# Performance work log

Measured on AMD Instinct MI355X. Metric: run time of the kernel, lower is better.

## Reference

```python
import jax, jax.numpy as jnp
import numpy as np

POOL = 7              # roi_size (output bins per side)
SAMPLING_RATIO = 2    # bilinear samples per bin side
POOLED_DIM = 5        # CEM_FILTER(245) // (7*7)
SPATIAL_SCALE = 0.0625  # 1/16 feature stride


def setup_inputs() -> dict:
    key = jax.random.key(0)
    k1, k2, k3 = jax.random.split(key, 3)
    B, C, H, W = 8, 245, 100, 100
    N = 512
    IMG = 1600.0
    x = jax.random.normal(k1, (B, C, H, W), dtype=jnp.float32)
    xy = jax.random.uniform(k2, (B, N, 2), minval=0.0, maxval=IMG - 256.0)
    wh = jax.random.uniform(k3, (B, N, 2), minval=16.0, maxval=256.0)
    boxes = jnp.concatenate([xy, xy + wh], axis=-1)  # (x1,y1,x2,y2) in image coords
    return {"x": x, "boxes": boxes}


def reference(x, boxes):
    """Position-sensitive RoIAlign (torchvision ps_roi_align semantics).
    x: [B, C=POOLED_DIM*POOL*POOL, H, W]; boxes: [B, N, 4] in image coords.
    Returns [B*N, POOLED_DIM, POOL, POOL]."""
    B, C, H, W = x.shape
    Bb, N, _ = boxes.shape
    R = Bb * N
    g, P, D, s = SAMPLING_RATIO, POOL, POOLED_DIM, SPATIAL_SCALE

    batch_idx = jnp.repeat(jnp.arange(Bb, dtype=jnp.int32), N)  # convert_to_roi_format ids
    rois = boxes.reshape(R, 4)

    # aligned roi coords on the feature map (half-pixel offset)
    start_w = rois[:, 0] * s - 0.5
    start_h = rois[:, 1] * s - 0.5
    end_w = rois[:, 2] * s - 0.5
    end_h = rois[:, 3] * s - 0.5
    bin_h = (end_h - start_h) / P
    bin_w = (end_w - start_w) / P

    p = jnp.arange(P, dtype=jnp.float32)
    i = jnp.arange(g, dtype=jnp.float32)
    # sample coordinates, shape [R, P, g]
    ys = start_h[:, None, None] + p[None, :, None] * bin_h[:, None, None] \
         + (i[None, None, :] + 0.5) * bin_h[:, None, None] / g
    xs = start_w[:, None, None] + p[None, :, None] * bin_w[:, None, None] \
         + (i[None, None, :] + 0.5) * bin_w[:, None, None] / g

    # zero outside [-1, H] / [-1, W] (torchvision bilinear_interpolate)
    vy = ((ys >= -1.0) & (ys <= H)).astype(x.dtype)  # [R,P,g]
    vx = ((xs >= -1.0) & (xs <= W)).astype(x.dtype)

    yc = jnp.clip(ys, 0.0, H - 1.0)
    xc = jnp.clip(xs, 0.0, W - 1.0)
    yl = jnp.floor(yc).astype(jnp.int32)
    xl = jnp.floor(xc).astype(jnp.int32)
    yh = jnp.minimum(yl + 1, H - 1)
    xh = jnp.minimum(xl + 1, W - 1)
    ly = yc - yl.astype(x.dtype); hy = 1.0 - ly
    lx = xc - xl.astype(x.dtype); hx = 1.0 - lx

    # position-sensitive input channel: c_in = (d*P + ph)*P + pw, shape [D,P,P]
    c_in = ((jnp.arange(D)[:, None, None] * P + jnp.arange(P)[None, :, None]) * P
            + jnp.arange(P)[None, None, :]).astype(jnp.int32)

    # broadcast to [R, D, P(h), P(w), g(h), g(w)]
    b = batch_idx[:, None, None, None, None, None]
    c = c_in[None, :, :, :, None, None]
    gy = lambda a: a[:, None, :, None, :, None]  # y-axis arrays [R,P,g]
    gx = lambda a: a[:, None, None, :, None, :]  # x-axis arrays [R,P,g]

    v11 = x[b, c, gy(yl), gx(xl)]
    v12 = x[b, c, gy(yl), gx(xh)]
    v21 = x[b, c, gy(yh), gx(xl)]
    v22 = x[b, c, gy(yh), gx(xh)]
    val = (gy(hy) * gx(hx) * v11 + gy(hy) * gx(lx) * v12
           + gy(ly) * gx(hx) * v21 + gy(ly) * gx(lx) * v22)
    val = val * (gy(vy) * gx(vx))
    out = val.sum(axis=(4, 5)) / (g * g)  # average over sampling grid -> [R, D, P, P]
    return out
```

## Files before the change

kernel.cpp:

```cpp
#include <hip/hip_runtime.h>

#define POOL 7
#define SCALE 0.0625f
#define HW 10000
#define NROI 512
#define NCH 245

typedef const __attribute__((address_space(1))) void* gas_ptr;
typedef __attribute__((address_space(3))) void* las_ptr;

__global__ __launch_bounds__(512) void psroi_kernel(
    const float* __restrict__ x, const float* __restrict__ boxes,
    float* __restrict__ out, int H, int W)
{
    __shared__ float plane[HW + 4];

    int bid = blockIdx.x;
    int b = bid & 7;
    int c = bid >> 3;
    int p = b * NCH + c;
    int ph = (c / POOL) % POOL;
    int pw = c % POOL;

    int n = threadIdx.x;
    int r = b * NROI + n;

    float4 bx = *(const float4*)(boxes + (size_t)r * 4);

    const float4* __restrict__ src4 = (const float4*)(x + (size_t)p * HW);
    int lane = threadIdx.x & 63;
    int wave = threadIdx.x >> 6;
    #pragma unroll
    for (int i = 0; i < 5; ++i) {
        int chunk_base = i * 512 + wave * 64;
        int chunk = chunk_base + lane;
        if (chunk < HW / 4) {
            __builtin_amdgcn_global_load_lds(
                (gas_ptr)(src4 + chunk),
                (las_ptr)((char*)plane + (size_t)chunk_base * 16),
                16, 0, 0);
        }
    }
    if (threadIdx.x < 4) plane[HW + threadIdx.x] = 0.f;

    float sw = bx.x * SCALE - 0.5f;
    float sh = bx.y * SCALE - 0.5f;
    float ew = bx.z * SCALE - 0.5f;
    float eh = bx.w * SCALE - 0.5f;
    float bin_h = (eh - sh) / (float)POOL;
    float bin_w = (ew - sw) / (float)POOL;
    float fy0 = sh + (float)ph * bin_h;
    float fx0 = sw + (float)pw * bin_w;

    int   rowa[2], rstep[2];
    float wyh[2], wyl[2];
    #pragma unroll
    for (int iy = 0; iy < 2; ++iy) {
        float y  = fy0 + ((float)iy + 0.5f) * bin_h * 0.5f;
        float vy = (y >= -1.0f && y <= (float)H) ? 1.0f : 0.0f;
        float yc = fminf(fmaxf(y, 0.0f), (float)(H - 1));
        int   yl = (int)floorf(yc);
        float ly = yc - (float)yl;
        wyl[iy] = ly * vy;
        wyh[iy] = (1.0f - ly) * vy;
        rowa[iy]  = yl * W;
        rstep[iy] = (yl < H - 1) ? W : 0;
    }
    int   colx[2];
    float wxh[2], wxl[2];
    #pragma unroll
    for (int ix = 0; ix < 2; ++ix) {
        float xf = fx0 + ((float)ix + 0.5f) * bin_w * 0.5f;
        float vx = (xf >= -1.0f && xf <= (float)W) ? 1.0f : 0.0f;
        float xc = fminf(fmaxf(xf, 0.0f), (float)(W - 1));
        int   xl = (int)floorf(xc);
        float lx = xc - (float)xl;
        wxl[ix] = lx * vx;
        wxh[ix] = (1.0f - lx) * vx;
        colx[ix] = xl;
    }

    __syncthreads();

    float sum = 0.f;
    #pragma unroll
    for (int iy = 0; iy < 2; ++iy) {
        #pragma unroll
        for (int ix = 0; ix < 2; ++ix) {
            int a0 = rowa[iy] + colx[ix];
            int a1 = a0 + rstep[iy];
            float v11 = plane[a0];
            float v12 = plane[a0 + 1];
            float v21 = plane[a1];
            float v22 = plane[a1 + 1];
            float top = wxh[ix] * v11 + wxl[ix] * v12;
            float bot = wxh[ix] * v21 + wxl[ix] * v22;
            sum = fmaf(wyh[iy], top, sum);
            sum = fmaf(wyl[iy], bot, sum);
        }
    }
    out[(size_t)r * NCH + c] = sum * 0.25f;
}

extern "C" void kernel_launch(void* const* d_in, const int* in_sizes, int n_in,
                              void* d_out, int out_size, void* d_ws, size_t ws_size,
                              hipStream_t stream) {
    const float* x     = (const float*)d_in[0];
    const float* boxes = (const float*)d_in[1];
    float* out = (float*)d_out;

    const int H = 100, W = 100;
    (void)in_sizes; (void)n_in; (void)out_size; (void)d_ws; (void)ws_size;

    hipLaunchKernelGGL(psroi_kernel, dim3(NCH * 8), dim3(512), 0, stream,
                       x, boxes, out, H, W);
}
```

Baseline: 19.20 us.

## Process several channel planes per block with double-buffered LDS staging

```diff
diff --git a/kernel.cpp b/kernel.cpp
--- a/kernel.cpp
+++ b/kernel.cpp
@@ -5,101 +5,121 @@
 #define HW 10000
 #define NROI 512
 #define NCH 245
+#define JJ 64
 
 typedef const __attribute__((address_space(1))) void* gas_ptr;
 typedef __attribute__((address_space(3))) void* las_ptr;
 
 __global__ __launch_bounds__(512) void psroi_kernel(
     const float* __restrict__ x, const float* __restrict__ boxes,
-    float* __restrict__ out, int H, int W)
+    float* __restrict__ out)
 {
-    __shared__ float plane[HW + 4];
+    __shared__ float plane[2][HW + 4];
 
+    const int H = 100, W = 100;
     int bid = blockIdx.x;
     int b = bid & 7;
-    int c = bid >> 3;
-    int p = b * NCH + c;
-    int ph = (c / POOL) % POOL;
-    int pw = c % POOL;
+    int j = bid >> 3;
+    int npl = (j < 53) ? 4 : 3;
 
     int n = threadIdx.x;
     int r = b * NROI + n;
+    int lane = threadIdx.x & 63;
+    int wave = threadIdx.x >> 6;
+
+    const float* xb = x + (size_t)b * NCH * HW;
+
+    auto stage = [&](int buf, int c) {
+        const float4* src4 = (const float4*)(xb + (size_t)c * HW);
+        #pragma unroll
+        for (int i = 0; i < 5; ++i) {
+            int chunk_base = i * 512 + wave * 64;
+            int chunk = chunk_base + lane;
+            if (chunk < HW / 4) {
+                __builtin_amdgcn_global_load_lds(
+                    (gas_ptr)(src4 + chunk),
+                    (las_ptr)((char*)&plane[buf][0] + (size_t)chunk_base * 16),
+                    16, 0, 0);
+            }
+        }
+    };
 
     float4 bx = *(const float4*)(boxes + (size_t)r * 4);
-
-    const float4* __restrict__ src4 = (const float4*)(x + (size_t)p * HW);
-    int lane = threadIdx.x & 63;
-    int wave = threadIdx.x >> 6;
-    #pragma unroll
-    for (int i = 0; i < 5; ++i) {
-        int chunk_base = i * 512 + wave * 64;
-        int chunk = chunk_base + lane;
-        if (chunk < HW / 4) {
-            __builtin_amdgcn_global_load_lds(
-                (gas_ptr)(src4 + chunk),
-                (las_ptr)((char*)plane + (size_t)chunk_base * 16),
-                16, 0, 0);
-        }
-    }
-    if (threadIdx.x < 4) plane[HW + threadIdx.x] = 0.f;
+    stage(0, j);
+    if (threadIdx.x < 8)
+        plane[threadIdx.x >> 2][HW + (threadIdx.x & 3)] = 0.f;
 
     float sw = bx.x * SCALE - 0.5f;
     float sh = bx.y * SCALE - 0.5f;
-    float ew = bx.z * SCALE - 0.5f;
-    float eh = bx.w * SCALE - 0.5f;
-    float bin_h = (eh - sh) / (float)POOL;
-    float bin_w = (ew - sw) / (float)POOL;
-    float fy0 = sh + (float)ph * bin_h;
-    float fx0 = sw + (float)pw * bin_w;
-
-    int   rowa[2], rstep[2];
-    float wyh[2], wyl[2];
-    #pragma unroll
-    for (int iy = 0; iy < 2; ++iy) {
-        float y  = fy0 + ((float)iy + 0.5f) * bin_h * 0.5f;
-        float vy = (y >= -1.0f && y <= (float)H) ? 1.0f : 0.0f;
-        float yc = fminf(fmaxf(y, 0.0f), (float)(H - 1));
-        int   yl = (int)floorf(yc);
-        float ly = yc - (float)yl;
-        wyl[iy] = ly * vy;
-        wyh[iy] = (1.0f - ly) * vy;
-        rowa[iy]  = yl * W;
-        rstep[iy] = (yl < H - 1) ? W : 0;
-    }
-    int   colx[2];
-    float wxh[2], wxl[2];
-    #pragma unroll
-    for (int ix = 0; ix < 2; ++ix) {
-        float xf = fx0 + ((float)ix + 0.5f) * bin_w * 0.5f;
-        float vx = (xf >= -1.0f && xf <= (float)W) ? 1.0f : 0.0f;
-        float xc = fminf(fmaxf(xf, 0.0f), (float)(W - 1));
-        int   xl = (int)floorf(xc);
-        float lx = xc - (float)xl;
-        wxl[ix] = lx * vx;
-        wxh[ix] = (1.0f - lx) * vx;
-        colx[ix] = xl;
-    }
+    float bin_h = (bx.w * SCALE - 0.5f - sh) / (float)POOL;
+    float bin_w = (bx.z * SCALE - 0.5f - sw) / (float)POOL;
 
     __syncthreads();
 
-    float sum = 0.f;
-    #pragma unroll
-    for (int iy = 0; iy < 2; ++iy) {
+    for (int t = 0; t < npl; ++t) {
+        int c = j + JJ * t;
+        bool pre = (t + 1 < npl);
+        if (pre) stage((t + 1) & 1, j + JJ * (t + 1));
+
+        int ph = (c / POOL) % POOL;
+        int pw = c % POOL;
+        float fy0 = sh + (float)ph * bin_h;
+        float fx0 = sw + (float)pw * bin_w;
+
+        int   rowa[2], rstep[2];
+        float wyh[2], wyl[2];
+        #pragma unroll
+        for (int iy = 0; iy < 2; ++iy) {
+            float y  = fy0 + ((float)iy + 0.5f) * bin_h * 0.5f;
+            float vy = (y >= -1.0f && y <= (float)H) ? 1.0f : 0.0f;
+            float yc = fminf(fmaxf(y, 0.0f), (float)(H - 1));
+            int   yl = (int)floorf(yc);
+            float ly = yc - (float)yl;
+            wyl[iy] = ly * vy;
+            wyh[iy] = (1.0f - ly) * vy;
+            rowa[iy]  = yl * W;
+            rstep[iy] = (yl < H - 1) ? W : 0;
+        }
+        int   colx[2];
+        float wxh[2], wxl[2];
         #pragma unroll
         for (int ix = 0; ix < 2; ++ix) {
-            int a0 = rowa[iy] + colx[ix];
-            int a1 = a0 + rstep[iy];
-            float v11 = plane[a0];
-            float v12 = plane[a0 + 1];
-            float v21 = plane[a1];
-            float v22 = plane[a1 + 1];
-            float top = wxh[ix] * v11 + wxl[ix] * v12;
-            float bot = wxh[ix] * v21 + wxl[ix] * v22;
-            sum = fmaf(wyh[iy], top, sum);
-            sum = fmaf(wyl[iy], bot, sum);
+            float xf = fx0 + ((float)ix + 0.5f) * bin_w * 0.5f;
+            float vx = (xf >= -1.0f && xf <= (float)W) ? 1.0f : 0.0f;
+            float xc = fminf(fmaxf(xf, 0.0f), (float)(W - 1));
+            int   xl = (int)floorf(xc);
+            float lx = xc - (float)xl;
+            wxl[ix] = lx * vx;
+            wxh[ix] = (1.0f - lx) * vx;
+            colx[ix] = xl;
         }
+
+        if (pre) asm volatile("s_waitcnt vmcnt(5)" ::: "memory");
+        else     asm volatile("s_waitcnt vmcnt(0)" ::: "memory");
+        __builtin_amdgcn_s_barrier();
+
+        const float* pl = &plane[t & 1][0];
+        float sum = 0.f;
+        #pragma unroll
+        for (int iy = 0; iy < 2; ++iy) {
+            #pragma unroll
+            for (int ix = 0; ix < 2; ++ix) {
+                int a0 = rowa[iy] + colx[ix];
+                int a1 = a0 + rstep[iy];
+                float v11 = pl[a0];
+                float v12 = pl[a0 + 1];
+                float v21 = pl[a1];
+                float v22 = pl[a1 + 1];
+                float top = wxh[ix] * v11 + wxl[ix] * v12;
+                float bot = wxh[ix] * v21 + wxl[ix] * v22;
+                sum = fmaf(wyh[iy], top, sum);
+                sum = fmaf(wyl[iy], bot, sum);
+            }
+        }
+        out[(size_t)r * NCH + c] = sum * 0.25f;
+
+        __builtin_amdgcn_s_barrier();
     }
-    out[(size_t)r * NCH + c] = sum * 0.25f;
 }
 
 extern "C" void kernel_launch(void* const* d_in, const int* in_sizes, int n_in,
@@ -109,9 +129,8 @@
     const float* boxes = (const float*)d_in[1];
     float* out = (float*)d_out;
 
-    const int H = 100, W = 100;
     (void)in_sizes; (void)n_in; (void)out_size; (void)d_ws; (void)ws_size;
 
-    hipLaunchKernelGGL(psroi_kernel, dim3(NCH * 8), dim3(512), 0, stream,
-                       x, boxes, out, H, W);
+    hipLaunchKernelGGL(psroi_kernel, dim3(8 * JJ), dim3(512), 0, stream,
+                       x, boxes, out);
 }
```

New measurement: 19.83 us. 3.3% more time.
